# Kernel optimization log

Hardware: AMD Instinct MI355X
Metric: run time of the kernel (lower is better)

## Reference

```python
import jax, jax.numpy as jnp
import numpy as np

HOMO_BOOST_THRD = 0.5
HOMO_LOSS_WEIGHT = 100.0
EPS = 1e-8  # F.cosine_similarity default eps

N_NODES = 50000
N_EDGES = 1600000
D_FEAT = 128
N_TARGET = 5000
N_BKD = 500


def setup_inputs() -> dict:
    key = jax.random.key(0)
    k1, k2, k3, k4, k5 = jax.random.split(key, 5)
    edge_index = jax.random.randint(k1, (2, N_EDGES), 0, N_NODES, dtype=jnp.int64 if jax.config.jax_enable_x64 else jnp.int32)
    edge_weights = jax.random.uniform(k2, (N_EDGES,), dtype=jnp.float32)
    x = jax.random.normal(k3, (N_NODES, D_FEAT), dtype=jnp.float32)
    target_nodes = jax.random.randint(k4, (N_TARGET,), 0, N_NODES)
    bkd_nodes = jax.random.randint(k5, (N_BKD,), 0, N_NODES)
    return {"edge_index": edge_index, "edge_weights": edge_weights, "x": x,
            "target_nodes": target_nodes, "bkd_nodes": bkd_nodes}


def reference(edge_index, edge_weights, x, target_nodes, bkd_nodes):
    n = x.shape[0]
    # membership bitmaps replace per-edge python `in set` checks
    is_bkd = jnp.zeros((n,), dtype=bool).at[bkd_nodes].set(True)
    is_tgt = jnp.zeros((n,), dtype=bool).at[target_nodes].set(True)

    u, v = edge_index[0], edge_index[1]
    # dense_to_sparse in the original drops zero-weight edges
    mask = ((is_bkd[u] & is_tgt[v]) | (is_bkd[v] & is_tgt[u])) & (edge_weights != 0)

    xu = x[u]  # [E, d]
    xv = x[v]  # [E, d]
    dot = jnp.sum(xu * xv, axis=-1)
    nu = jnp.maximum(jnp.linalg.norm(xu, axis=-1), EPS)
    nv = jnp.maximum(jnp.linalg.norm(xv, axis=-1), EPS)
    sims = dot / (nu * nv)  # F.cosine_similarity

    per_edge = jnp.maximum(HOMO_BOOST_THRD - sims, 0.0)  # clamp-at-zero branch
    loss = HOMO_LOSS_WEIGHT * jnp.sum(jnp.where(mask, per_edge, 0.0))
    return loss
```

## Files before the change

### kernel.cpp

```cpp
#include <hip/hip_runtime.h>

#define HOMO_BOOST_THRD 0.5f
#define HOMO_LOSS_WEIGHT 100.0f
#define COS_EPS 1e-8f
#define D_FEAT 128
#define EDGE_BLOCK 256
#define EPT 8

#define FLAG_WORDS_MAX 4096

__global__ __launch_bounds__(EDGE_BLOCK) void edge_loss_kernel(
        const int* __restrict__ edge_index,
        const float* __restrict__ edge_weights,
        const float* __restrict__ x,
        const int* __restrict__ target_nodes, int n_tgt,
        const int* __restrict__ bkd_nodes, int n_bkd,
        float* __restrict__ partials, int E, int nwords) {
    __shared__ unsigned int sflags[FLAG_WORDS_MAX];

    uint4* s4 = reinterpret_cast<uint4*>(sflags);
    const int nwords4 = (nwords + 3) >> 2;
    for (int i = threadIdx.x; i < nwords4; i += EDGE_BLOCK)
        s4[i] = make_uint4(0u, 0u, 0u, 0u);
    __syncthreads();

    const int n_tgt4 = n_tgt >> 2;
    const int4* t4 = reinterpret_cast<const int4*>(target_nodes);
    for (int i = threadIdx.x; i < n_tgt4; i += EDGE_BLOCK) {
        int4 nd = t4[i];
        atomicOr(&sflags[nd.x >> 4], 2u << ((nd.x & 15) * 2));
        atomicOr(&sflags[nd.y >> 4], 2u << ((nd.y & 15) * 2));
        atomicOr(&sflags[nd.z >> 4], 2u << ((nd.z & 15) * 2));
        atomicOr(&sflags[nd.w >> 4], 2u << ((nd.w & 15) * 2));
    }
    for (int i = (n_tgt4 << 2) + threadIdx.x; i < n_tgt; i += EDGE_BLOCK) {
        int node = target_nodes[i];
        atomicOr(&sflags[node >> 4], 2u << ((node & 15) * 2));
    }
    const int n_bkd4 = n_bkd >> 2;
    const int4* b4 = reinterpret_cast<const int4*>(bkd_nodes);
    for (int i = threadIdx.x; i < n_bkd4; i += EDGE_BLOCK) {
        int4 nd = b4[i];
        atomicOr(&sflags[nd.x >> 4], 1u << ((nd.x & 15) * 2));
        atomicOr(&sflags[nd.y >> 4], 1u << ((nd.y & 15) * 2));
        atomicOr(&sflags[nd.z >> 4], 1u << ((nd.z & 15) * 2));
        atomicOr(&sflags[nd.w >> 4], 1u << ((nd.w & 15) * 2));
    }
    for (int i = (n_bkd4 << 2) + threadIdx.x; i < n_bkd; i += EDGE_BLOCK) {
        int node = bkd_nodes[i];
        atomicOr(&sflags[node >> 4], 1u << ((node & 15) * 2));
    }
    __syncthreads();

    const int lane = threadIdx.x & 63;
    const int base = (blockIdx.x * EDGE_BLOCK + threadIdx.x) * EPT;
    const int wave_base = (blockIdx.x * EDGE_BLOCK + (threadIdx.x & ~63)) * EPT;
    const bool full = (wave_base + 64 * EPT <= E) && ((E & 3) == 0);

    int us[EPT], vs[EPT];
    if (full) {
        const int4* up = reinterpret_cast<const int4*>(edge_index + base);
        const int4* vp = reinterpret_cast<const int4*>(edge_index + E + base);
        #pragma unroll
        for (int q = 0; q < EPT / 4; ++q) {
            int4 uq = up[q];
            int4 vq = vp[q];
            us[q*4+0] = uq.x; us[q*4+1] = uq.y; us[q*4+2] = uq.z; us[q*4+3] = uq.w;
            vs[q*4+0] = vq.x; vs[q*4+1] = vq.y; vs[q*4+2] = vq.z; vs[q*4+3] = vq.w;
        }
    } else {
        #pragma unroll
        for (int k = 0; k < EPT; ++k) {
            int e = base + k;
            bool ok = (e < E);
            us[k] = ok ? edge_index[e] : 0;
            vs[k] = ok ? edge_index[E + e] : 0;
        }
    }

    float wval = 0.0f;

    #pragma unroll
    for (int k = 0; k < EPT; ++k) {
        bool valid = full || (base + k < E);
        unsigned fu = (sflags[us[k] >> 4] >> ((us[k] & 15) * 2)) & 3u;
        unsigned fv = (sflags[vs[k] >> 4] >> ((vs[k] & 15) * 2)) & 3u;
        bool m = valid && ((((fu & (fv >> 1)) | (fv & (fu >> 1))) & 1u) != 0);

        unsigned long long mb = __ballot(m);
        while (mb) {
            int b = __ffsll(mb) - 1;
            mb &= mb - 1;
            int eu = __shfl(us[k], b, 64);
            int ev = __shfl(vs[k], b, 64);
            int e_b = wave_base + b * EPT + k;
            float w = edge_weights[e_b];
            if (w != 0.0f) {
                float2 a = reinterpret_cast<const float2*>(x + (size_t)eu * D_FEAT)[lane];
                float2 c = reinterpret_cast<const float2*>(x + (size_t)ev * D_FEAT)[lane];
                float d  = a.x * c.x + a.y * c.y;
                float p  = a.x * a.x + a.y * a.y;
                float q  = c.x * c.x + c.y * c.y;
                #pragma unroll
                for (int off = 1; off < 64; off <<= 1) {
                    d += __shfl_xor(d, off, 64);
                    p += __shfl_xor(p, off, 64);
                    q += __shfl_xor(q, off, 64);
                }
                float nu = fmaxf(sqrtf(p), COS_EPS);
                float nv = fmaxf(sqrtf(q), COS_EPS);
                float term = fmaxf(HOMO_BOOST_THRD - d / (nu * nv), 0.0f);
                if (lane == 0) wval += term;
            }
        }
    }

    if (lane == 0)
        partials[blockIdx.x * (EDGE_BLOCK / 64) + (threadIdx.x >> 6)] = wval;
}

__global__ void reduce_kernel(const float* __restrict__ partials, int n,
                              float* __restrict__ out) {
    __shared__ float wsum[16];
    float s = 0.0f;
    for (int i = threadIdx.x; i < n; i += blockDim.x) s += partials[i];
    #pragma unroll
    for (int off = 32; off > 0; off >>= 1) s += __shfl_down(s, off, 64);
    if ((threadIdx.x & 63) == 0) wsum[threadIdx.x >> 6] = s;
    __syncthreads();
    if (threadIdx.x == 0) {
        float t = 0.0f;
        for (int w = 0; w < (int)(blockDim.x >> 6); ++w) t += wsum[w];
        out[0] = t * HOMO_LOSS_WEIGHT;
    }
}

extern "C" void kernel_launch(void* const* d_in, const int* in_sizes, int n_in,
                              void* d_out, int out_size, void* d_ws, size_t ws_size,
                              hipStream_t stream) {
    const int*   edge_index   = (const int*)  d_in[0];
    const float* edge_weights = (const float*)d_in[1];
    const float* x            = (const float*)d_in[2];
    const int*   target_nodes = (const int*)  d_in[3];
    const int*   bkd_nodes    = (const int*)  d_in[4];

    const int E     = in_sizes[0] / 2;
    const int N     = in_sizes[2] / D_FEAT;
    const int n_tgt = in_sizes[3];
    const int n_bkd = in_sizes[4];

    const int nwords = (N + 15) / 16;
    float* partials = (float*)d_ws;

    const int nblocks = (E + EDGE_BLOCK * EPT - 1) / (EDGE_BLOCK * EPT);
    edge_loss_kernel<<<nblocks, EDGE_BLOCK, 0, stream>>>(
        edge_index, edge_weights, x, target_nodes, n_tgt, bkd_nodes, n_bkd,
        partials, E, nwords);

    const int nwaves = nblocks * (EDGE_BLOCK / 64);
    reduce_kernel<<<1, 1024, 0, stream>>>(partials, nwaves, (float*)d_out);
}
```

Measured before the change: 14.92 us.

## Compact masked edges into shared queue and process two per wave

Rather than each wave looping over its own ballot of masked edges, every thread appends its masked, nonzero-weight edges to a block-level shared-memory queue via atomicAdd. The four waves then split the queue evenly, each handling two edges per iteration so more gather loads are in flight. The edge-weight load now happens per candidate thread before enqueueing. Partials are reduced per block, which shrinks the final reduction. This adds 16KB of shared memory plus an extra barrier, which may lower occupancy.

```diff
diff --git a/kernel.cpp b/kernel.cpp
--- a/kernel.cpp
+++ b/kernel.cpp
@@ -6,6 +6,7 @@
 #define D_FEAT 128
 #define EDGE_BLOCK 256
 #define EPT 8
+#define QMAX (EDGE_BLOCK * EPT)
 
 #define FLAG_WORDS_MAX 4096
 
@@ -17,11 +18,16 @@
         const int* __restrict__ bkd_nodes, int n_bkd,
         float* __restrict__ partials, int E, int nwords) {
     __shared__ unsigned int sflags[FLAG_WORDS_MAX];
+    __shared__ int q_u[QMAX];
+    __shared__ int q_v[QMAX];
+    __shared__ int qn;
+    __shared__ float wsum[EDGE_BLOCK / 64];
 
     uint4* s4 = reinterpret_cast<uint4*>(sflags);
     const int nwords4 = (nwords + 3) >> 2;
     for (int i = threadIdx.x; i < nwords4; i += EDGE_BLOCK)
         s4[i] = make_uint4(0u, 0u, 0u, 0u);
+    if (threadIdx.x == 0) qn = 0;
     __syncthreads();
 
     const int n_tgt4 = n_tgt >> 2;
@@ -52,21 +58,20 @@
     }
     __syncthreads();
 
-    const int lane = threadIdx.x & 63;
     const int base = (blockIdx.x * EDGE_BLOCK + threadIdx.x) * EPT;
-    const int wave_base = (blockIdx.x * EDGE_BLOCK + (threadIdx.x & ~63)) * EPT;
-    const bool full = (wave_base + 64 * EPT <= E) && ((E & 3) == 0);
+    const bool full = (blockIdx.x * EDGE_BLOCK * EPT + EDGE_BLOCK * EPT <= E)
+                      && ((E & 3) == 0);
 
     int us[EPT], vs[EPT];
     if (full) {
         const int4* up = reinterpret_cast<const int4*>(edge_index + base);
         const int4* vp = reinterpret_cast<const int4*>(edge_index + E + base);
         #pragma unroll
-        for (int q = 0; q < EPT / 4; ++q) {
-            int4 uq = up[q];
-            int4 vq = vp[q];
-            us[q*4+0] = uq.x; us[q*4+1] = uq.y; us[q*4+2] = uq.z; us[q*4+3] = uq.w;
-            vs[q*4+0] = vq.x; vs[q*4+1] = vq.y; vs[q*4+2] = vq.z; vs[q*4+3] = vq.w;
+        for (int qd = 0; qd < EPT / 4; ++qd) {
+            int4 uq = up[qd];
+            int4 vq = vp[qd];
+            us[qd*4+0] = uq.x; us[qd*4+1] = uq.y; us[qd*4+2] = uq.z; us[qd*4+3] = uq.w;
+            vs[qd*4+0] = vq.x; vs[qd*4+1] = vq.y; vs[qd*4+2] = vq.z; vs[qd*4+3] = vq.w;
         }
     } else {
         #pragma unroll
@@ -78,45 +83,70 @@
         }
     }
 
-    float wval = 0.0f;
-
     #pragma unroll
     for (int k = 0; k < EPT; ++k) {
         bool valid = full || (base + k < E);
         unsigned fu = (sflags[us[k] >> 4] >> ((us[k] & 15) * 2)) & 3u;
         unsigned fv = (sflags[vs[k] >> 4] >> ((vs[k] & 15) * 2)) & 3u;
         bool m = valid && ((((fu & (fv >> 1)) | (fv & (fu >> 1))) & 1u) != 0);
+        if (m) {
+            float w = edge_weights[base + k];
+            if (w != 0.0f) {
+                int qi = atomicAdd(&qn, 1);
+                q_u[qi] = us[k];
+                q_v[qi] = vs[k];
+            }
+        }
+    }
+    __syncthreads();
 
-        unsigned long long mb = __ballot(m);
-        while (mb) {
-            int b = __ffsll(mb) - 1;
-            mb &= mb - 1;
-            int eu = __shfl(us[k], b, 64);
-            int ev = __shfl(vs[k], b, 64);
-            int e_b = wave_base + b * EPT + k;
-            float w = edge_weights[e_b];
-            if (w != 0.0f) {
-                float2 a = reinterpret_cast<const float2*>(x + (size_t)eu * D_FEAT)[lane];
-                float2 c = reinterpret_cast<const float2*>(x + (size_t)ev * D_FEAT)[lane];
-                float d  = a.x * c.x + a.y * c.y;
-                float p  = a.x * a.x + a.y * a.y;
-                float q  = c.x * c.x + c.y * c.y;
-                #pragma unroll
-                for (int off = 1; off < 64; off <<= 1) {
-                    d += __shfl_xor(d, off, 64);
-                    p += __shfl_xor(p, off, 64);
-                    q += __shfl_xor(q, off, 64);
-                }
-                float nu = fmaxf(sqrtf(p), COS_EPS);
-                float nv = fmaxf(sqrtf(q), COS_EPS);
-                float term = fmaxf(HOMO_BOOST_THRD - d / (nu * nv), 0.0f);
-                if (lane == 0) wval += term;
+    const int lane = threadIdx.x & 63;
+    const int wid  = threadIdx.x >> 6;
+    const int nq   = qn;
+    float wval = 0.0f;
+
+    for (int i = wid * 2; i < nq; i += 2 * (EDGE_BLOCK / 64)) {
+        bool has1 = (i + 1 < nq);
+        int u0 = q_u[i], v0 = q_v[i];
+        int u1 = has1 ? q_u[i + 1] : u0;
+        int v1 = has1 ? q_v[i + 1] : v0;
+
+        float2 a0 = reinterpret_cast<const float2*>(x + (size_t)u0 * D_FEAT)[lane];
+        float2 c0 = reinterpret_cast<const float2*>(x + (size_t)v0 * D_FEAT)[lane];
+        float2 a1 = reinterpret_cast<const float2*>(x + (size_t)u1 * D_FEAT)[lane];
+        float2 c1 = reinterpret_cast<const float2*>(x + (size_t)v1 * D_FEAT)[lane];
+
+        float d0 = a0.x * c0.x + a0.y * c0.y;
+        float p0 = a0.x * a0.x + a0.y * a0.y;
+        float q0 = c0.x * c0.x + c0.y * c0.y;
+        float d1 = a1.x * c1.x + a1.y * c1.y;
+        float p1 = a1.x * a1.x + a1.y * a1.y;
+        float q1 = c1.x * c1.x + c1.y * c1.y;
+        #pragma unroll
+        for (int off = 1; off < 64; off <<= 1) {
+            d0 += __shfl_xor(d0, off, 64);
+            p0 += __shfl_xor(p0, off, 64);
+            q0 += __shfl_xor(q0, off, 64);
+            d1 += __shfl_xor(d1, off, 64);
+            p1 += __shfl_xor(p1, off, 64);
+            q1 += __shfl_xor(q1, off, 64);
+        }
+        if (lane == 0) {
+            float nu0 = fmaxf(sqrtf(p0), COS_EPS);
+            float nv0 = fmaxf(sqrtf(q0), COS_EPS);
+            wval += fmaxf(HOMO_BOOST_THRD - d0 / (nu0 * nv0), 0.0f);
+            if (has1) {
+                float nu1 = fmaxf(sqrtf(p1), COS_EPS);
+                float nv1 = fmaxf(sqrtf(q1), COS_EPS);
+                wval += fmaxf(HOMO_BOOST_THRD - d1 / (nu1 * nv1), 0.0f);
             }
         }
     }
 
-    if (lane == 0)
-        partials[blockIdx.x * (EDGE_BLOCK / 64) + (threadIdx.x >> 6)] = wval;
+    if (lane == 0) wsum[wid] = wval;
+    __syncthreads();
+    if (threadIdx.x == 0)
+        partials[blockIdx.x] = wsum[0] + wsum[1] + wsum[2] + wsum[3];
 }
 
 __global__ void reduce_kernel(const float* __restrict__ partials, int n,
@@ -157,6 +187,5 @@
         edge_index, edge_weights, x, target_nodes, n_tgt, bkd_nodes, n_bkd,
         partials, E, nwords);
 
-    const int nwaves = nblocks * (EDGE_BLOCK / 64);
-    reduce_kernel<<<1, 1024, 0, stream>>>(partials, nwaves, (float*)d_out);
+    reduce_kernel<<<1, 1024, 0, stream>>>(partials, nblocks, (float*)d_out);
 }
```

After: 13.58 us. -9.0%, faster.
